# Performance work log

Measured on AMD Instinct MI355X. Metric: run time of the kernel, lower is better.

## Reference

```python
import jax, jax.numpy as jnp
import numpy as np

ALPHA = 1.0


def _lstm(seq, w_ih, w_hh, b_ih, b_hh):
    # seq: [T, B, F]; PyTorch gate order i, f, g, o
    B = seq.shape[1]
    H = w_hh.shape[1]
    h0 = jnp.zeros((B, H), seq.dtype)

    def step(carry, xt):
        h, c = carry
        g = xt @ w_ih.T + h @ w_hh.T + b_ih + b_hh
        i, f, gg, o = jnp.split(g, 4, axis=-1)
        c = jax.nn.sigmoid(f) * c + jax.nn.sigmoid(i) * jnp.tanh(gg)
        h = jax.nn.sigmoid(o) * jnp.tanh(c)
        return (h, c), h

    _, hs = jax.lax.scan(step, (h0, h0), seq)
    return hs  # [T, B, H]


def setup_inputs() -> dict:
    key = jax.random.key(0)
    ks = jax.random.split(key, 16)
    B, T, F = 128, 8192, 10
    F1, H1, H2, K = 8, 8, 7, 16
    s = lambda k, shp: jax.random.normal(k, shp, jnp.float32) * 0.1
    return {
        "x": jax.random.normal(ks[0], (B, T, F), jnp.float32),
        "conv_w": s(ks[1], (F1, F)),      # Conv1d k=1: [out, in]
        "conv_b": s(ks[2], (F1,)),
        "w_ih1": s(ks[3], (4 * H1, F1)),
        "w_hh1": s(ks[4], (4 * H1, H1)),
        "b_ih1": s(ks[5], (4 * H1,)),
        "b_hh1": s(ks[6], (4 * H1,)),
        "w_ih2": s(ks[7], (4 * H2, H1)),
        "w_hh2": s(ks[8], (4 * H2, H2)),
        "b_ih2": s(ks[9], (4 * H2,)),
        "b_hh2": s(ks[10], (4 * H2,)),
        "dec_w": s(ks[11], (H2, F)),      # ConvTranspose1d k=1: [in, out]
        "dec_b": s(ks[12], (F,)),
        "centers": jax.random.uniform(ks[13], (K, H2), jnp.float32, -0.5, 0.5),
    }


def reference(x, conv_w, conv_b, w_ih1, w_hh1, b_ih1, b_hh1,
              w_ih2, w_hh2, b_ih2, b_hh2, dec_w, dec_b, centers):
    # ---- TAE encoder ----
    h = jax.nn.leaky_relu(jnp.einsum('btf,of->bto', x, conv_w) + conv_b, 0.01)
    seq = jnp.transpose(h, (1, 0, 2))                       # [T, B, F1]
    h1 = jnp.tanh(_lstm(seq, w_ih1, w_hh1, b_ih1, b_hh1))   # [T, B, H1]
    z = jnp.tanh(_lstm(h1, w_ih2, w_hh2, b_ih2, b_hh2))     # [T, B, H2]
    z = jnp.transpose(z, (1, 0, 2))                         # [B, T, H2]
    # ---- TAE decoder (ConvTranspose1d, kernel 1) ----
    x_reconstr = jnp.einsum('btc,cf->btf', z, dec_w) + dec_b
    # ---- batched soft cluster assignment (original loops per sample) ----
    # squared euclidean distance to centroids: [B, T, K]
    sim = (jnp.sum(z * z, -1, keepdims=True)
           + jnp.sum(centers * centers, -1)
           - 2.0 * jnp.einsum('btc,kc->btk', z, centers))
    Q = jnp.power(1.0 + sim / ALPHA, -(ALPHA + 1.0) / 2.0)
    fq = Q / jnp.sum(Q, axis=2, keepdims=True)              # row-normalize over K
    P = (Q * Q) / jnp.sum(Q, axis=1, keepdims=True)         # column sums over T (per sample)
    fp = P / jnp.sum(P, axis=2, keepdims=True)
    return z, x_reconstr, fp, fq
```

## Files before the change

kernel.cpp:

```cpp
#include <hip/hip_runtime.h>
#include <cstdint>
#include <cstddef>

#define B_ 128
#define T_ 8192
#define F_ 10
#define F1_ 8
#define H1_ 8
#define H2_ 7
#define K_ 16
#define CHUNK 64
#define NC (T_/CHUNK)

#define LOG2E 1.4426950408889634f

__device__ __forceinline__ float exp2_fast(float x){ float r; asm("v_exp_f32 %0, %1" : "=v"(r) : "v"(x)); return r; }
__device__ __forceinline__ float rcp_fast(float x){ float r; asm("v_rcp_f32 %0, %1" : "=v"(r) : "v"(x)); return r; }
template<int CTRL>
__device__ __forceinline__ float dppf(float x){
  return __int_as_float(__builtin_amdgcn_update_dpp(0, __float_as_int(x), CTRL, 0xF, 0xF, true));
}
#define ROR(m) (0x120+(m))
#define WIDX(u,m) (((u)+8-(m))&7)
__device__ __forceinline__ float ror8(float x){ return dppf<0x128>(x); }
typedef int v2i_t __attribute__((ext_vector_type(2)));

__global__ __launch_bounds__(320,1) void k2_lstm(
    const float* __restrict__ x,
    const float* __restrict__ conv_w, const float* __restrict__ conv_b,
    const float* __restrict__ w_ih1, const float* __restrict__ b_ih1,
    const float* __restrict__ b_hh1, const float* __restrict__ w_hh1,
    const float* __restrict__ w_ih2, const float* __restrict__ w_hh2,
    const float* __restrict__ b_ih2, const float* __restrict__ b_hh2,
    const float* __restrict__ centers,
    const float* __restrict__ dec_w, const float* __restrict__ dec_b,
    float* __restrict__ zout, float* __restrict__ xrg,
    float* __restrict__ fqg, float* __restrict__ Sws)
{
  __shared__ float h1r[2*CHUNK*64];
  __shared__ float ffr[2*CHUNK*64];
  __shared__ float h2r[2*CHUNK*64];
  __shared__ float g1r[2*CHUNK*32];
  __shared__ float esc[64];
  const int b = blockIdx.x;
  const int tid = threadIdx.x;
  const int wv = tid >> 6;
  const int lane = tid & 63;
  const int u = lane & 7;
  const bool c2 = (lane >> 3) & 1;
  const bool up = (lane >> 5) & 1;
  const bool isg = (c2 && !up);
  const float A2 = isg ? (-2.f*LOG2E) : 0.5f;
  const float D_ = isg ? ( 2.f*LOG2E) : 0.f;
  const float Sx = isg ? (-2.f*LOG2E) : (-LOG2E);

  if (wv == 1){
    const int prow = u + (c2 ? 16 : 0) + (up ? 8 : 0);
    float wp[8];
    #pragma unroll
    for (int m=0;m<8;++m) wp[m] = w_hh1[prow*8 + WIDX(u,m)] * Sx;
    float hq=0.f, csq=0.f;
    for (int k=0;k<NC+4;++k){
      if (k>=1 && k<NC+1){
        const int ck = k-1;
        const float* g1p = &g1r[(ck&1)*CHUNK*32];
        float* hp = &h1r[(ck&1)*CHUNK*64];
        float fpf[8];
        #pragma unroll
        for (int i=0;i<8;++i) fpf[i] = g1p[i*32 + prow];
        for (int s0=0;s0<CHUNK;s0+=8){
          #pragma unroll
          for (int si=0;si<8;++si){
            const int s = s0+si;
            float pre = fpf[si];
            int rp = s+8; if (rp>CHUNK-1) rp = CHUNK-1;
            fpf[si] = g1p[rp*32 + prow];
            float x1 = dppf<ROR(1)>(hq);
            float x2 = dppf<ROR(2)>(hq);
            float x3 = dppf<ROR(3)>(hq);
            float x4 = dppf<ROR(4)>(hq);
            float x5 = dppf<ROR(5)>(hq);
            float x6 = dppf<ROR(6)>(hq);
            float x7 = dppf<ROR(7)>(hq);
            float A0 = fmaf(wp[0], hq, pre);
            A0 = fmaf(wp[4], x4, A0);
            float p2 = wp[2]*x2;
            float p3 = wp[3]*x3;
            A0 = fmaf(wp[1], x1, A0);
            float P2 = fmaf(wp[6], x6, p2);
            float P3 = fmaf(wp[7], x7, p3);
            float p5 = wp[5]*x5;
            A0 = A0 + p5;
            float g = A0 + (P2+P3);
            float e = exp2_fast(g);
            float tg = fmaf(e, 0.5f, 0.5f);
            float r = rcp_fast(tg);
            float y = fmaf(A2, r, D_);
            v2i_t pr = __builtin_amdgcn_permlane32_swap(__float_as_int(y), __float_as_int(y), false, false);
            float lov = __int_as_float(pr.x);
            float hiv = __int_as_float(pr.y);
            float IG = lov * ror8(lov);
            float HR = ror8(hiv);
            float Fv = c2 ? HR : hiv;
            float Ov = c2 ? hiv : HR;
            float cs = fmaf(Fv, csq, IG);
            float e2 = exp2_fast(cs);
            float t2 = fmaf(e2, 0.5f, 0.5f);
            float r2v = rcp_fast(t2);
            float hn = fmaf(Ov, r2v, -Ov);
            csq = cs; hq = hn;
            hp[(s<<6)+lane] = hn;
          }
        }
      }
      asm volatile("s_waitcnt lgkmcnt(0)\ns_barrier" ::: "memory");
    }
  } else if (wv == 2){
    const int r2 = u + (c2 ? 14 : 0) + (up ? 7 : 0);
    float wb[8];
    #pragma unroll
    for (int m=0;m<8;++m) wb[m] = 0.f;
    if (u < 7){
      #pragma unroll
      for (int m=0;m<8;++m){
        int jm = WIDX(u,m);
        wb[m] = (jm<7) ? w_hh2[r2*7+jm]*Sx : 0.f;
      }
    }
    float hq=0.f, csq=0.f;
    for (int k=0;k<NC+4;++k){
      if (k>=3 && k<NC+3){
        const int ck = k-3;
        const float* fp_ = &ffr[(ck&1)*CHUNK*64];
        float* hp = &h2r[(ck&1)*CHUNK*64];
        float4 cA = *(const float4*)&fp_[(lane<<3)];
        float4 cB = *(const float4*)&fp_[(lane<<3)+4];
        for (int j=0;j<8;++j){
          const int jn = (j<7) ? j+1 : 7;
          float4 nA = *(const float4*)&fp_[(jn<<9)+(lane<<3)];
          float4 nB = *(const float4*)&fp_[(jn<<9)+(lane<<3)+4];
          #pragma unroll
          for (int si=0;si<8;++si){
            const int s = (j<<3)+si;
            float ffv = (si<4) ? (&cA.x)[si] : (&cB.x)[si-4];
            float x1 = dppf<ROR(1)>(hq);
            float x2 = dppf<ROR(2)>(hq);
            float x3 = dppf<ROR(3)>(hq);
            float x4 = dppf<ROR(4)>(hq);
            float x5 = dppf<ROR(5)>(hq);
            float x6 = dppf<ROR(6)>(hq);
            float x7 = dppf<ROR(7)>(hq);
            float A0 = fmaf(wb[0], hq, ffv);
            A0 = fmaf(wb[4], x4, A0);
            float p2 = wb[2]*x2;
            float p3 = wb[3]*x3;
            A0 = fmaf(wb[1], x1, A0);
            float P2 = fmaf(wb[6], x6, p2);
            float P3 = fmaf(wb[7], x7, p3);
            float p5 = wb[5]*x5;
            A0 = A0 + p5;
            float g = A0 + (P2+P3);
            float e = exp2_fast(g);
            float tg = fmaf(e, 0.5f, 0.5f);
            float r = rcp_fast(tg);
            float y = fmaf(A2, r, D_);
            v2i_t pr = __builtin_amdgcn_permlane32_swap(__float_as_int(y), __float_as_int(y), false, false);
            float lov = __int_as_float(pr.x);
            float hiv = __int_as_float(pr.y);
            float IG = lov * ror8(lov);
            float HR = ror8(hiv);
            float Fv = c2 ? HR : hiv;
            float Ov = c2 ? hiv : HR;
            float cs = fmaf(Fv, csq, IG);
            float e2 = exp2_fast(cs);
            float t2 = fmaf(e2, 0.5f, 0.5f);
            float r2v = rcp_fast(t2);
            float hn = fmaf(Ov, r2v, -Ov);
            csq = cs; hq = hn;
            hp[(s<<6)+lane] = hn;
          }
          cA = nA; cB = nB;
        }
      }
      asm volatile("s_waitcnt lgkmcnt(0)\ns_barrier" ::: "memory");
    }
  } else if (wv == 0){
    const int r2 = u + (c2 ? 14 : 0) + (up ? 7 : 0);
    float wff[8]; float pre2C = 0.f;
    #pragma unroll
    for (int m=0;m<8;++m) wff[m] = 0.f;
    if (u < 7){
      #pragma unroll
      for (int m=0;m<8;++m) wff[m] = w_ih2[r2*8 + WIDX(u,m)] * Sx;
      pre2C = (b_ih2[r2]+b_hh2[r2])*Sx;
    }
    for (int k=0;k<NC+4;++k){
      if (k>=2 && k<NC+2){
        const int ck = k-2;
        const float* h1p = &h1r[(ck&1)*CHUNK*64];
        float* ffp = &ffr[(ck&1)*CHUNK*64];
        for (int s0=0;s0<CHUNK;s0+=8){
          #pragma unroll
          for (int si=0;si<8;++si){
            const int s = s0+si;
            float hv = h1p[(s<<6)+lane];
            float e3 = exp2_fast(hv * (-2.f*LOG2E));
            float t3 = fmaf(e3, 0.5f, 0.5f);
            float th = rcp_fast(t3) - 1.f;
            float f1 = dppf<ROR(1)>(th);
            float f2 = dppf<ROR(2)>(th);
            float f3 = dppf<ROR(3)>(th);
            float f4 = dppf<ROR(4)>(th);
            float f5 = dppf<ROR(5)>(th);
            float f6 = dppf<ROR(6)>(th);
            float f7 = dppf<ROR(7)>(th);
            float F0 = fmaf(wff[0], th, pre2C);
            F0 = fmaf(wff[4], f4, F0);
            float q2 = wff[2]*f2;
            float q3 = wff[3]*f3;
            F0 = fmaf(wff[1], f1, F0);
            q2 = fmaf(wff[6], f6, q2);
            q3 = fmaf(wff[7], f7, q3);
            float q5 = wff[5]*f5;
            F0 = F0 + q5;
            float ffv = F0 + (q2+q3);
            ffp[((s0>>3)<<9) + (lane<<3) + si] = ffv;
          }
        }
      }
      asm volatile("s_waitcnt lgkmcnt(0)\ns_barrier" ::: "memory");
    }
  } else if (wv == 3){
    const int kk = lane & 15;
    float ckp[8]; float accS = 0.f;
    #pragma unroll
    for (int m=0;m<8;++m){
      int j = WIDX(u,m);
      ckp[m] = (j<7) ? centers[kk*H2_ + j] : 0.f;
    }
    float dw[8]; float xb = 0.f;
    #pragma unroll
    for (int m=0;m<8;++m){
      int j = WIDX(u,m);
      dw[m] = (j<7 && kk<10) ? dec_w[j*F_ + kk] : 0.f;
    }
    if (kk < 10) xb = dec_b[kk];
    float* zb = zout + (size_t)b*T_*H2_;
    float* fqb = fqg + (size_t)b*T_*K_;
    float* xrb = xrg + (size_t)b*T_*F_;
    const int srow = lane >> 3;
    const int fr = lane >> 4;
    for (int k=0;k<NC+4;++k){
      if (k>=4 && k<NC+4){
        const int ck = k-4;
        const float* h2p = &h2r[(ck&1)*CHUNK*64];
        const int base_t = ck*CHUNK;
        for (int s0=0;s0<CHUNK;s0+=8){
          float zs[8], fqv[8], xv[8];
          #pragma unroll
          for (int si=0;si<8;++si){
            float hv = h2p[((s0+si)<<6)+lane];
            float e3 = exp2_fast(hv * (-2.f*LOG2E));
            float t3 = fmaf(e3, 0.5f, 0.5f);
            float z = rcp_fast(t3) - 1.f;
            zs[si] = z;
            float z1 = dppf<ROR(1)>(z);
            float z2 = dppf<ROR(2)>(z);
            float z3 = dppf<ROR(3)>(z);
            float z4 = dppf<ROR(4)>(z);
            float z5 = dppf<ROR(5)>(z);
            float z6 = dppf<ROR(6)>(z);
            float z7 = dppf<ROR(7)>(z);
            float d = 1.f;
            float t0 = z  - ckp[0]; d = fmaf(t0,t0,d);
            float u1 = z1 - ckp[1]; d = fmaf(u1,u1,d);
            float u2 = z2 - ckp[2]; d = fmaf(u2,u2,d);
            float u3 = z3 - ckp[3]; d = fmaf(u3,u3,d);
            float u4 = z4 - ckp[4]; d = fmaf(u4,u4,d);
            float u5 = z5 - ckp[5]; d = fmaf(u5,u5,d);
            float u6 = z6 - ckp[6]; d = fmaf(u6,u6,d);
            float u7 = z7 - ckp[7]; d = fmaf(u7,u7,d);
            float Qv = rcp_fast(d);
            accS += Qv;
            float t1r = Qv + dppf<0x128>(Qv);
            float t2r = t1r + dppf<0x124>(t1r);
            float t3r = t2r + dppf<0x122>(t2r);
            float qsv = t3r + dppf<0x121>(t3r);
            fqv[si] = Qv * rcp_fast(qsv);
            float xo = xb;
            xo = fmaf(dw[0], z , xo);
            xo = fmaf(dw[1], z1, xo);
            xo = fmaf(dw[2], z2, xo);
            xo = fmaf(dw[3], z3, xo);
            xo = fmaf(dw[4], z4, xo);
            xo = fmaf(dw[5], z5, xo);
            xo = fmaf(dw[6], z6, xo);
            xo = fmaf(dw[7], z7, xo);
            xv[si] = xo;
          }
          float v0 = ((lane>>3)&1) ? zs[1] : zs[0];
          float v1 = ((lane>>3)&1) ? zs[3] : zs[2];
          float v2 = ((lane>>3)&1) ? zs[5] : zs[4];
          float v3 = ((lane>>3)&1) ? zs[7] : zs[6];
          float w0 = ((lane>>4)&1) ? v1 : v0;
          float w1 = ((lane>>4)&1) ? v3 : v2;
          float zo = ((lane>>5)&1) ? w1 : w0;
          if (u < 7) zb[(size_t)(base_t + s0 + srow)*H2_ + u] = zo;
          float a0 = (lane&16)? fqv[1]:fqv[0];
          float a1 = (lane&16)? fqv[3]:fqv[2];
          float vA = (lane&32)? a1:a0;
          float b0 = (lane&16)? fqv[5]:fqv[4];
          float b1 = (lane&16)? fqv[7]:fqv[6];
          float vB = (lane&32)? b1:b0;
          fqb[(size_t)(base_t+s0+fr)*K_ + kk] = vA;
          fqb[(size_t)(base_t+s0+4+fr)*K_ + kk] = vB;
          float c0 = (lane&16)? xv[1]:xv[0];
          float c1 = (lane&16)? xv[3]:xv[2];
          float xA = (lane&32)? c1:c0;
          float d0 = (lane&16)? xv[5]:xv[4];
          float d1 = (lane&16)? xv[7]:xv[6];
          float xB = (lane&32)? d1:d0;
          if (kk < 10){
            xrb[(size_t)(base_t+s0+fr)*F_ + kk] = xA;
            xrb[(size_t)(base_t+s0+4+fr)*F_ + kk] = xB;
          }
        }
      }
      asm volatile("s_waitcnt lgkmcnt(0)\ns_barrier" ::: "memory");
    }
    if (lane < 16) Sws[b*K_ + lane] = accS;
  } else {
    const int sg = lane >> 3;
    float cw[F_];
    #pragma unroll
    for (int f=0;f<F_;++f) cw[f] = conv_w[u*F_+f];
    const float cb = conv_b[u];
    float wi[4][8], bi[4];
    #pragma unroll
    for (int q=0;q<4;++q){
      const int row = q*8+u;
      const float Sq = (q==2)? (-2.f*LOG2E) : (-LOG2E);
      #pragma unroll
      for (int j=0;j<8;++j) wi[q][j] = w_ih1[row*F1_+j]*Sq;
      bi[q] = (b_ih1[row]+b_hh1[row])*Sq;
    }
    const float* xbp = x + (size_t)b*T_*F_;
    for (int k=0;k<NC+4;++k){
      if (k < NC){
        float* gp = &g1r[(k&1)*CHUNK*32];
        for (int p=0;p<8;++p){
          const int s = p*8+sg;
          const float2* xp = (const float2*)(xbp + (size_t)(k*CHUNK+s)*F_);
          float2 xv0=xp[0], xv1=xp[1], xv2=xp[2], xv3=xp[3], xv4=xp[4];
          float enc = cb;
          enc = fmaf(cw[0],xv0.x,enc); enc = fmaf(cw[1],xv0.y,enc);
          enc = fmaf(cw[2],xv1.x,enc); enc = fmaf(cw[3],xv1.y,enc);
          enc = fmaf(cw[4],xv2.x,enc); enc = fmaf(cw[5],xv2.y,enc);
          enc = fmaf(cw[6],xv3.x,enc); enc = fmaf(cw[7],xv3.y,enc);
          enc = fmaf(cw[8],xv4.x,enc); enc = fmaf(cw[9],xv4.y,enc);
          enc = enc > 0.f ? enc : 0.01f*enc;
          esc[(sg<<3)+u] = enc;
          float4 eA = *(const float4*)&esc[sg<<3];
          float4 eB = *(const float4*)&esc[(sg<<3)+4];
          #pragma unroll
          for (int q=0;q<4;++q){
            float pq = bi[q];
            pq = fmaf(wi[q][0],eA.x,pq); pq = fmaf(wi[q][1],eA.y,pq);
            pq = fmaf(wi[q][2],eA.z,pq); pq = fmaf(wi[q][3],eA.w,pq);
            pq = fmaf(wi[q][4],eB.x,pq); pq = fmaf(wi[q][5],eB.y,pq);
            pq = fmaf(wi[q][6],eB.z,pq); pq = fmaf(wi[q][7],eB.w,pq);
            gp[s*32 + q*8 + u] = pq;
          }
        }
      }
      asm volatile("s_waitcnt lgkmcnt(0)\ns_barrier" ::: "memory");
    }
  }
}

__global__ __launch_bounds__(256) void k4_fp(const float* __restrict__ zout,
    const float* __restrict__ centers, const float* __restrict__ Sws,
    float* __restrict__ fp)
{
  int idx = blockIdx.x*256 + threadIdx.x;
  if (idx >= B_*T_) return;
  int b = idx >> 13;
  float zv[H2_]; float zz=0.f;
  const float* zp = zout + (size_t)idx*H2_;
  #pragma unroll
  for (int j=0;j<H2_;++j){ zv[j]=zp[j]; zz+=zv[j]*zv[j]; }
  float P[K_]; float ps=0.f;
  #pragma unroll
  for (int k=0;k<K_;++k){
    float d = zz;
    #pragma unroll
    for (int j=0;j<H2_;++j){ float c=centers[k*H2_+j]; d += c*c - 2.f*c*zv[j]; }
    float q = rcp_fast(1.f+d);
    float p = q*q*rcp_fast(Sws[b*K_+k]);
    P[k]=p; ps+=p;
  }
  float ip = rcp_fast(ps);
  float4* fpp = (float4*)(fp + (size_t)idx*K_);
  #pragma unroll
  for (int c=0;c<4;++c){
    float4 vp;
    vp.x=P[4*c+0]*ip; vp.y=P[4*c+1]*ip; vp.z=P[4*c+2]*ip; vp.w=P[4*c+3]*ip;
    fpp[c]=vp;
  }
}

extern "C" void kernel_launch(void* const* d_in, const int* in_sizes, int n_in,
                              void* d_out, int out_size, void* d_ws, size_t ws_size,
                              hipStream_t stream)
{
  (void)in_sizes; (void)n_in; (void)out_size; (void)ws_size;
  const float* x      = (const float*)d_in[0];
  const float* conv_w = (const float*)d_in[1];
  const float* conv_b = (const float*)d_in[2];
  const float* w_ih1  = (const float*)d_in[3];
  const float* w_hh1  = (const float*)d_in[4];
  const float* b_ih1  = (const float*)d_in[5];
  const float* b_hh1  = (const float*)d_in[6];
  const float* w_ih2  = (const float*)d_in[7];
  const float* w_hh2  = (const float*)d_in[8];
  const float* b_ih2  = (const float*)d_in[9];
  const float* b_hh2  = (const float*)d_in[10];
  const float* dec_w  = (const float*)d_in[11];
  const float* dec_b  = (const float*)d_in[12];
  const float* centers= (const float*)d_in[13];

  float* out = (float*)d_out;
  float* z   = out;
  float* xr  = out + (size_t)B_*T_*H2_;
  float* fp  = xr  + (size_t)B_*T_*F_;
  float* fq  = fp  + (size_t)B_*T_*K_;

  float* Sws = (float*)d_ws;

  k2_lstm<<<dim3(B_), dim3(320), 0, stream>>>(x, conv_w, conv_b,
      w_ih1, b_ih1, b_hh1, w_hh1, w_ih2, w_hh2, b_ih2, b_hh2,
      centers, dec_w, dec_b, z, xr, fq, Sws);
  k4_fp<<<dim3((B_*T_)/256), dim3(256), 0, stream>>>(z, centers, Sws, fp);
}
```

Before: 943.8 us.

## Move fq and decoder output to epilogue kernel; transpose gate-input LDS layout

The fq normalization and ConvTranspose decoder computation move out of the serial LSTM kernel's output wave into the fully parallel epilogue kernel, which now writes xr, fp and fq. The output wave keeps only the z write and the column-sum accumulation. Separately, the layer-1 gate pre-activation buffer is stored transposed so the recurrent wave can fetch eight timesteps per row with two float4 LDS reads instead of per-step scalar reads. The aim is to shorten the critical path of the latency-bound 128-block LSTM kernel, at the cost of the epilogue recomputing the distances and carrying more global traffic.

```diff
diff --git a/kernel.cpp b/kernel.cpp
--- a/kernel.cpp
+++ b/kernel.cpp
@@ -33,9 +33,7 @@
     const float* __restrict__ w_ih2, const float* __restrict__ w_hh2,
     const float* __restrict__ b_ih2, const float* __restrict__ b_hh2,
     const float* __restrict__ centers,
-    const float* __restrict__ dec_w, const float* __restrict__ dec_b,
-    float* __restrict__ zout, float* __restrict__ xrg,
-    float* __restrict__ fqg, float* __restrict__ Sws)
+    float* __restrict__ zout, float* __restrict__ Sws)
 {
   __shared__ float h1r[2*CHUNK*64];
   __shared__ float ffr[2*CHUNK*64];
@@ -65,16 +63,16 @@
         const int ck = k-1;
         const float* g1p = &g1r[(ck&1)*CHUNK*32];
         float* hp = &h1r[(ck&1)*CHUNK*64];
-        float fpf[8];
-        #pragma unroll
-        for (int i=0;i<8;++i) fpf[i] = g1p[i*32 + prow];
-        for (int s0=0;s0<CHUNK;s0+=8){
+        float4 cA = *(const float4*)&g1p[(prow<<3)];
+        float4 cB = *(const float4*)&g1p[(prow<<3)+4];
+        for (int j=0;j<8;++j){
+          const int jn = (j<7) ? j+1 : 7;
+          float4 nA = *(const float4*)&g1p[(jn<<8)+(prow<<3)];
+          float4 nB = *(const float4*)&g1p[(jn<<8)+(prow<<3)+4];
           #pragma unroll
           for (int si=0;si<8;++si){
-            const int s = s0+si;
-            float pre = fpf[si];
-            int rp = s+8; if (rp>CHUNK-1) rp = CHUNK-1;
-            fpf[si] = g1p[rp*32 + prow];
+            const int s = (j<<3)+si;
+            float pre = (si<4) ? (&cA.x)[si] : (&cB.x)[si-4];
             float x1 = dppf<ROR(1)>(hq);
             float x2 = dppf<ROR(2)>(hq);
             float x3 = dppf<ROR(3)>(hq);
@@ -111,6 +109,7 @@
             csq = cs; hq = hn;
             hp[(s<<6)+lane] = hn;
           }
+          cA = nA; cB = nB;
         }
       }
       asm volatile("s_waitcnt lgkmcnt(0)\ns_barrier" ::: "memory");
@@ -238,25 +237,15 @@
       int j = WIDX(u,m);
       ckp[m] = (j<7) ? centers[kk*H2_ + j] : 0.f;
     }
-    float dw[8]; float xb = 0.f;
-    #pragma unroll
-    for (int m=0;m<8;++m){
-      int j = WIDX(u,m);
-      dw[m] = (j<7 && kk<10) ? dec_w[j*F_ + kk] : 0.f;
-    }
-    if (kk < 10) xb = dec_b[kk];
     float* zb = zout + (size_t)b*T_*H2_;
-    float* fqb = fqg + (size_t)b*T_*K_;
-    float* xrb = xrg + (size_t)b*T_*F_;
     const int srow = lane >> 3;
-    const int fr = lane >> 4;
     for (int k=0;k<NC+4;++k){
       if (k>=4 && k<NC+4){
         const int ck = k-4;
         const float* h2p = &h2r[(ck&1)*CHUNK*64];
         const int base_t = ck*CHUNK;
         for (int s0=0;s0<CHUNK;s0+=8){
-          float zs[8], fqv[8], xv[8];
+          float zs[8];
           #pragma unroll
           for (int si=0;si<8;++si){
             float hv = h2p[((s0+si)<<6)+lane];
@@ -280,23 +269,7 @@
             float u5 = z5 - ckp[5]; d = fmaf(u5,u5,d);
             float u6 = z6 - ckp[6]; d = fmaf(u6,u6,d);
             float u7 = z7 - ckp[7]; d = fmaf(u7,u7,d);
-            float Qv = rcp_fast(d);
-            accS += Qv;
-            float t1r = Qv + dppf<0x128>(Qv);
-            float t2r = t1r + dppf<0x124>(t1r);
-            float t3r = t2r + dppf<0x122>(t2r);
-            float qsv = t3r + dppf<0x121>(t3r);
-            fqv[si] = Qv * rcp_fast(qsv);
-            float xo = xb;
-            xo = fmaf(dw[0], z , xo);
-            xo = fmaf(dw[1], z1, xo);
-            xo = fmaf(dw[2], z2, xo);
-            xo = fmaf(dw[3], z3, xo);
-            xo = fmaf(dw[4], z4, xo);
-            xo = fmaf(dw[5], z5, xo);
-            xo = fmaf(dw[6], z6, xo);
-            xo = fmaf(dw[7], z7, xo);
-            xv[si] = xo;
+            accS += rcp_fast(d);
           }
           float v0 = ((lane>>3)&1) ? zs[1] : zs[0];
           float v1 = ((lane>>3)&1) ? zs[3] : zs[2];
@@ -306,24 +279,6 @@
           float w1 = ((lane>>4)&1) ? v3 : v2;
           float zo = ((lane>>5)&1) ? w1 : w0;
           if (u < 7) zb[(size_t)(base_t + s0 + srow)*H2_ + u] = zo;
-          float a0 = (lane&16)? fqv[1]:fqv[0];
-          float a1 = (lane&16)? fqv[3]:fqv[2];
-          float vA = (lane&32)? a1:a0;
-          float b0 = (lane&16)? fqv[5]:fqv[4];
-          float b1 = (lane&16)? fqv[7]:fqv[6];
-          float vB = (lane&32)? b1:b0;
-          fqb[(size_t)(base_t+s0+fr)*K_ + kk] = vA;
-          fqb[(size_t)(base_t+s0+4+fr)*K_ + kk] = vB;
-          float c0 = (lane&16)? xv[1]:xv[0];
-          float c1 = (lane&16)? xv[3]:xv[2];
-          float xA = (lane&32)? c1:c0;
-          float d0 = (lane&16)? xv[5]:xv[4];
-          float d1 = (lane&16)? xv[7]:xv[6];
-          float xB = (lane&32)? d1:d0;
-          if (kk < 10){
-            xrb[(size_t)(base_t+s0+fr)*F_ + kk] = xA;
-            xrb[(size_t)(base_t+s0+4+fr)*F_ + kk] = xB;
-          }
         }
       }
       asm volatile("s_waitcnt lgkmcnt(0)\ns_barrier" ::: "memory");
@@ -369,7 +324,7 @@
             pq = fmaf(wi[q][2],eA.z,pq); pq = fmaf(wi[q][3],eA.w,pq);
             pq = fmaf(wi[q][4],eB.x,pq); pq = fmaf(wi[q][5],eB.y,pq);
             pq = fmaf(wi[q][6],eB.z,pq); pq = fmaf(wi[q][7],eB.w,pq);
-            gp[s*32 + q*8 + u] = pq;
+            gp[(p<<8) + ((q*8+u)<<3) + sg] = pq;
           }
         }
       }
@@ -378,9 +333,10 @@
   }
 }
 
-__global__ __launch_bounds__(256) void k4_fp(const float* __restrict__ zout,
+__global__ __launch_bounds__(256) void k4_out(const float* __restrict__ zout,
+    const float* __restrict__ dec_w, const float* __restrict__ dec_b,
     const float* __restrict__ centers, const float* __restrict__ Sws,
-    float* __restrict__ fp)
+    float* __restrict__ xr, float* __restrict__ fp, float* __restrict__ fq)
 {
   int idx = blockIdx.x*256 + threadIdx.x;
   if (idx >= B_*T_) return;
@@ -389,23 +345,38 @@
   const float* zp = zout + (size_t)idx*H2_;
   #pragma unroll
   for (int j=0;j<H2_;++j){ zv[j]=zp[j]; zz+=zv[j]*zv[j]; }
-  float P[K_]; float ps=0.f;
+  float2 xo[5];
+  #pragma unroll
+  for (int f=0; f<F_; ++f){
+    float a = dec_b[f];
+    #pragma unroll
+    for (int c=0;c<H2_;++c) a += zv[c]*dec_w[c*F_+f];
+    (&xo[0].x)[f] = a;
+  }
+  float2* xp2 = (float2*)(xr + (size_t)idx*F_);
+  #pragma unroll
+  for (int c=0;c<5;++c) xp2[c] = xo[c];
+
+  float Q[K_], P[K_]; float qs=0.f, ps=0.f;
   #pragma unroll
   for (int k=0;k<K_;++k){
     float d = zz;
     #pragma unroll
     for (int j=0;j<H2_;++j){ float c=centers[k*H2_+j]; d += c*c - 2.f*c*zv[j]; }
     float q = rcp_fast(1.f+d);
+    Q[k]=q; qs+=q;
     float p = q*q*rcp_fast(Sws[b*K_+k]);
     P[k]=p; ps+=p;
   }
-  float ip = rcp_fast(ps);
+  float iq = rcp_fast(qs), ip = rcp_fast(ps);
+  float4* fqp = (float4*)(fq + (size_t)idx*K_);
   float4* fpp = (float4*)(fp + (size_t)idx*K_);
   #pragma unroll
   for (int c=0;c<4;++c){
-    float4 vp;
+    float4 vq, vp;
+    vq.x=Q[4*c+0]*iq; vq.y=Q[4*c+1]*iq; vq.z=Q[4*c+2]*iq; vq.w=Q[4*c+3]*iq;
     vp.x=P[4*c+0]*ip; vp.y=P[4*c+1]*ip; vp.z=P[4*c+2]*ip; vp.w=P[4*c+3]*ip;
-    fpp[c]=vp;
+    fqp[c]=vq; fpp[c]=vp;
   }
 }
 
@@ -439,6 +410,7 @@
 
   k2_lstm<<<dim3(B_), dim3(320), 0, stream>>>(x, conv_w, conv_b,
       w_ih1, b_ih1, b_hh1, w_hh1, w_ih2, w_hh2, b_ih2, b_hh2,
-      centers, dec_w, dec_b, z, xr, fq, Sws);
-  k4_fp<<<dim3((B_*T_)/256), dim3(256), 0, stream>>>(z, centers, Sws, fp);
+      centers, z, Sws);
+  k4_out<<<dim3((B_*T_)/256), dim3(256), 0, stream>>>(z, dec_w, dec_b,
+      centers, Sws, xr, fp, fq);
 }
```

Measured after the change: 762.6 us. 1.24x faster.
